# Kernel tuning notes

Hardware: AMD Instinct MI355X
Metric: run time of the kernel (lower is better)

## Reference

```python
import jax, jax.numpy as jnp
import numpy as np

LAM = 5.0
NUM_STEPS = 100
B, N, D = 8, 1024, 256


def setup_inputs() -> dict:
    key = jax.random.key(0)
    k1, k2 = jax.random.split(key)
    fA = jax.random.normal(k1, (B, N, D), dtype=jnp.float32)
    fB = jax.random.normal(k2, (B, N, D), dtype=jnp.float32)
    dustbin = jnp.zeros((1,), dtype=jnp.float32)  # learned dustbin score, init 0.0
    return {"fA": fA, "fB": fB, "dustbin": dustbin}


def _l2_normalize(x, eps=1e-12):
    # matches tf.math.l2_normalize: x / sqrt(max(sum(x^2), eps))
    return x * jax.lax.rsqrt(jnp.maximum(jnp.sum(x * x, axis=-1, keepdims=True), eps))


def _forward(fA, fB, dustbin):
    b, n, _ = fA.shape
    fA = _l2_normalize(fA)
    fB = _l2_normalize(fB)
    Sij = jnp.einsum('bnd,bmd->bnm', fA, fB)  # (B, N, N)
    # augment with dustbin row/col -> (B, N+1, N+1)
    row = dustbin * jnp.ones((b, 1, n), Sij.dtype)
    col = dustbin * jnp.ones((b, n + 1, 1), Sij.dtype)
    S_aug = jnp.concatenate([jnp.concatenate([Sij, row], axis=1), col], axis=2)
    Cij = jnp.clip(-S_aug, -15.0 / LAM, 15.0 / LAM)
    # marginals: [1,...,1, N] for both rows and cols
    ab = jnp.concatenate([jnp.ones((n,), Sij.dtype), jnp.full((1,), float(n), Sij.dtype)])[None, :]  # (1, N+1)
    P = jnp.exp(-LAM * Cij)
    P = P / jnp.sum(P, axis=(1, 2), keepdims=True)

    def step(P, _):
        # NOTE: row_sum/col_sum both computed from the SAME P, as in the TF code
        row_sum = jnp.sum(P, axis=1)  # (B, N+1)
        col_sum = jnp.sum(P, axis=2)  # (B, N+1)
        P = P * (ab / col_sum)[:, :, None]
        P = P * (ab / row_sum)[:, None, :]
        return P, None

    P, _ = jax.lax.scan(jax.checkpoint(step), P, None, length=NUM_STEPS)
    return P


def reference(fA, fB, dustbin):
    return _forward(fA, fB, dustbin)
```

## Files before the change

### kernel.cpp

```cpp
#include <hip/hip_runtime.h>
#include <math.h>
#include <stdint.h>

#define NB 8
#define NN 1024
#define DD 256
#define NP1 1025
#define LDC 1028
#define NSTEPS 100

__global__ __launch_bounds__(256) void norm_kernel(const float* __restrict__ fA,
                                                   const float* __restrict__ fB,
                                                   float* __restrict__ invA,
                                                   float* __restrict__ invB) {
  int gw = (blockIdx.x * 256 + threadIdx.x) >> 6;
  int lane = threadIdx.x & 63;
  const float* src;
  float* dst;
  int row;
  if (gw < NB * NN) { src = fA; dst = invA; row = gw; }
  else              { src = fB; dst = invB; row = gw - NB * NN; }
  float4 v = *(const float4*)(src + (size_t)row * DD + lane * 4);
  double ss = (double)v.x * v.x + (double)v.y * v.y + (double)v.z * v.z + (double)v.w * v.w;
#pragma unroll
  for (int o = 32; o; o >>= 1) ss += __shfl_xor(ss, o, 64);
  if (lane == 0) dst[row] = (float)(1.0 / sqrt(fmax(ss, 1e-12)));
}

__global__ __launch_bounds__(256) void gemm_exp_kernel(const float* __restrict__ fA,
                                                       const float* __restrict__ fB,
                                                       const float* __restrict__ invA,
                                                       const float* __restrict__ invB,
                                                       float* __restrict__ P0,
                                                       double* __restrict__ partZ) {
  const int id = blockIdx.x;
  const int b = id & 7;
  const int tile = id >> 3;
  const int bx = tile & 15, by = tile >> 4;
  const int row0 = by * 64, col0 = bx * 64;
  const int tid = threadIdx.x;
  const int tx = tid & 15, ty = tid >> 4;
  __shared__ __align__(16) float As[16][68];
  __shared__ __align__(16) float Bs[16][68];
  __shared__ double zred[256];
  float acc[4][4] = {{0.f}};
  const int lm = tid >> 2, kq = (tid & 3) << 2;
  const float sa = invA[b * NN + row0 + lm];
  const float sb = invB[b * NN + col0 + lm];
  const float* pA = fA + (size_t)(b * NN + row0 + lm) * DD + kq;
  const float* pB = fB + (size_t)(b * NN + col0 + lm) * DD + kq;
  for (int k0 = 0; k0 < DD; k0 += 16) {
    const float4 a4 = *(const float4*)(pA + k0);
    const float4 b4 = *(const float4*)(pB + k0);
    As[kq + 0][lm] = a4.x * sa; As[kq + 1][lm] = a4.y * sa;
    As[kq + 2][lm] = a4.z * sa; As[kq + 3][lm] = a4.w * sa;
    Bs[kq + 0][lm] = b4.x * sb; Bs[kq + 1][lm] = b4.y * sb;
    Bs[kq + 2][lm] = b4.z * sb; Bs[kq + 3][lm] = b4.w * sb;
    __syncthreads();
#pragma unroll
    for (int kk = 0; kk < 16; ++kk) {
      const float4 av = *(const float4*)&As[kk][ty * 4];
      const float4 bv = *(const float4*)&Bs[kk][tx * 4];
      const float ar[4] = {av.x, av.y, av.z, av.w};
      const float br[4] = {bv.x, bv.y, bv.z, bv.w};
#pragma unroll
      for (int a = 0; a < 4; ++a)
#pragma unroll
        for (int e = 0; e < 4; ++e)
          acc[a][e] = fmaf(ar[a], br[e], acc[a][e]);
    }
    __syncthreads();
  }
  double zs = 0.0;
#pragma unroll
  for (int a = 0; a < 4; ++a)
#pragma unroll
    for (int e = 0; e < 4; ++e) {
      const float S = acc[a][e];
      const float C = fminf(fmaxf(-S, -3.0f), 3.0f);
      const float p = expf(-5.0f * C);
      acc[a][e] = p;
      zs += (double)p;
    }
  {
    float* P0b = P0 + (size_t)b * NN * NN;
#pragma unroll
    for (int a = 0; a < 4; ++a) {
      float4 v;
      v.x = acc[a][0]; v.y = acc[a][1]; v.z = acc[a][2]; v.w = acc[a][3];
      *(float4*)(P0b + (size_t)(row0 + ty * 4 + a) * NN + col0 + tx * 4) = v;
    }
  }
  zred[tid] = zs;
  __syncthreads();
#pragma unroll
  for (int o = 128; o; o >>= 1) {
    if (tid < o) zred[tid] += zred[tid + o];
    __syncthreads();
  }
  if (tid == 0) partZ[(b * 16 + by) * 16 + bx] = zred[0];
}

__global__ __launch_bounds__(256) void init_rc_kernel(const double* __restrict__ partZ,
                                                      float* __restrict__ r0,
                                                      double* __restrict__ Binit,
                                                      double* __restrict__ Bzero) {
  const int b = blockIdx.x, tid = threadIdx.x;
  __shared__ double red[256];
  red[tid] = partZ[b * 256 + tid];
  __syncthreads();
#pragma unroll
  for (int o = 128; o; o >>= 1) {
    if (tid < o) red[tid] += red[tid + o];
    __syncthreads();
  }
  const double Z = red[0];
  const float rv = (float)(1.0 / Z);
  for (int i = tid; i < NP1; i += 256) {
    r0[b * NP1 + i] = rv;
    Binit[b * NP1 + i] = (i == NN) ? (double)NN : 1.0;
    Bzero[b * NP1 + i] = 0.0;
  }
}

__global__ __launch_bounds__(512, 4) void step_kernel(const float* __restrict__ P0,
                                                      const float* __restrict__ dustbin,
                                                      const float* __restrict__ rin,
                                                      float* __restrict__ rout,
                                                      const double* __restrict__ Bprev,
                                                      double* __restrict__ Bacc,
                                                      double* __restrict__ Bzero) {
  const int id = blockIdx.x;
  const int b = id & 7;
  const int s = id >> 3;
  const int tid = threadIdx.x;
  const int lane = tid & 63;
  const int wv = tid >> 6;
  const bool desig = (s == 63);

  __shared__ __align__(16) float c_f[NN];
  __shared__ __align__(16) float part_lds[8][NN];
  __shared__ double wredR[8];
  __shared__ double wredC[8];
  __shared__ double cN_sh;

  const float d = dustbin[0];
  const float dv = expf(-5.0f * fminf(fmaxf(-d, -3.0f), 3.0f));
  const double dv_d = (double)dv;

  const float* P0b = P0 + (size_t)b * NN * NN;
  const float* rv_in = rin + b * NP1;
  const int rowA = s * 16 + wv;
  const int rowB = rowA + 8;
  const float wA = rv_in[rowA];
  const float wB = rv_in[rowB];
  const float4* pA4 = (const float4*)(P0b + (size_t)rowA * NN);
  const float4* pB4 = (const float4*)(P0b + (size_t)rowB * NN);

  float4 a4[4], b4[4];
#pragma unroll
  for (int k = 0; k < 4; ++k) {
    a4[k] = pA4[lane + (k << 6)];
    b4[k] = pB4[lane + (k << 6)];
  }

  if (tid < 17) {
    const int idx = id * 17 + tid;
    if (idx < NB * NP1) Bzero[idx] = 0.0;
  }
  const double* Bp = Bprev + b * NP1;
  for (int j = tid; j < NN; j += 512) c_f[j] = (float)(1.0 / Bp[j]);
  if (tid == 0) cN_sh = (double)NN / Bp[NN];
  __syncthreads();
  const double cN = cN_sh;

  double dotA = 0.0, dotB = 0.0;
  float4 pk[4];
#pragma unroll
  for (int k = 0; k < 4; ++k) {
    const int j4 = lane + (k << 6);
    const float4 cc = ((const float4*)c_f)[j4];
    dotA += (double)a4[k].x * (double)cc.x + (double)a4[k].y * (double)cc.y +
            (double)a4[k].z * (double)cc.z + (double)a4[k].w * (double)cc.w;
    dotB += (double)b4[k].x * (double)cc.x + (double)b4[k].y * (double)cc.y +
            (double)b4[k].z * (double)cc.z + (double)b4[k].w * (double)cc.w;
    pk[k].x = fmaf(wA, a4[k].x, wB * b4[k].x);
    pk[k].y = fmaf(wA, a4[k].y, wB * b4[k].y);
    pk[k].z = fmaf(wA, a4[k].z, wB * b4[k].z);
    pk[k].w = fmaf(wA, a4[k].w, wB * b4[k].w);
  }
#pragma unroll
  for (int o = 32; o; o >>= 1) {
    dotA += __shfl_xor(dotA, o, 64);
    dotB += __shfl_xor(dotB, o, 64);
  }
  dotA += dv_d * cN;
  dotB += dv_d * cN;
  if (lane == 0) {
    float* ro = rout + b * NP1;
    ro[rowA] = (float)(1.0 / dotA);
    ro[rowB] = (float)(1.0 / dotB);
    wredR[wv] = (double)wA + (double)wB;
  }
  {
    float4* pl4 = (float4*)&part_lds[wv][0];
#pragma unroll
    for (int k = 0; k < 4; ++k) pl4[lane + (k << 6)] = pk[k];
  }
  {
    double cs = (double)c_f[tid] + (double)c_f[tid + 512];
#pragma unroll
    for (int o = 32; o; o >>= 1) cs += __shfl_xor(cs, o, 64);
    if (lane == 0) wredC[wv] = cs;
  }
  __syncthreads();

  const float rN = rv_in[NN];
  const float rNdv = rN * dv;
  double* Ba = Bacc + b * NP1;
  for (int j = tid; j < NN; j += 512) {
    float s0 = ((part_lds[0][j] + part_lds[1][j]) + (part_lds[2][j] + part_lds[3][j])) +
               ((part_lds[4][j] + part_lds[5][j]) + (part_lds[6][j] + part_lds[7][j]));
    if (desig) s0 += rNdv;
    atomicAdd(Ba + j, (double)s0);
  }
  if (tid == 0) {
    double rsum = ((wredR[0] + wredR[1]) + (wredR[2] + wredR[3])) +
                  ((wredR[4] + wredR[5]) + (wredR[6] + wredR[7]));
    if (desig) rsum += (double)rN;
    atomicAdd(Ba + NN, dv_d * rsum);
    if (desig) {
      const double sc = ((wredC[0] + wredC[1]) + (wredC[2] + wredC[3])) +
                        ((wredC[4] + wredC[5]) + (wredC[6] + wredC[7])) + cN;
      rout[b * NP1 + NN] = (float)((double)NN / (dv_d * sc));
    }
  }
}

__global__ __launch_bounds__(256) void cfinal_kernel(const double* __restrict__ Bfin,
                                                     float* __restrict__ cfin) {
  const int b = blockIdx.x;
  for (int j = threadIdx.x; j < NP1; j += 256)
    cfin[b * LDC + j] = (float)(((j == NN) ? (double)NN : 1.0) / Bfin[b * NP1 + j]);
}

__global__ __launch_bounds__(256) void finalize_kernel(const float* __restrict__ P0,
                                                       const float* __restrict__ dustbin,
                                                       float* __restrict__ Pout,
                                                       const float* __restrict__ rfin,
                                                       const float* __restrict__ cfin) {
  const int bi = blockIdx.x;
  const int b = bi & 7, i = bi >> 3;
  const int tid = threadIdx.x;
  const float d = dustbin[0];
  const float dv = expf(-5.0f * fminf(fmaxf(-d, -3.0f), 3.0f));
  const float4* cv = (const float4*)(cfin + b * LDC);
  const float cN = cfin[b * LDC + NN];
  float* dst = Pout + (size_t)b * NP1 * NP1 + (size_t)i * NP1;
  const float4 c = cv[tid];
  if (i < NN) {
    const float rv = rfin[b * NP1 + i];
    const float4 p = ((const float4*)(P0 + ((size_t)b * NN + i) * NN))[tid];
    dst[tid * 4 + 0] = rv * p.x * c.x;
    dst[tid * 4 + 1] = rv * p.y * c.y;
    dst[tid * 4 + 2] = rv * p.z * c.z;
    dst[tid * 4 + 3] = rv * p.w * c.w;
    if (tid == 0) dst[NN] = rv * dv * cN;
  } else {
    const float rv = rfin[b * NP1 + NN];
    dst[tid * 4 + 0] = rv * dv * c.x;
    dst[tid * 4 + 1] = rv * dv * c.y;
    dst[tid * 4 + 2] = rv * dv * c.z;
    dst[tid * 4 + 3] = rv * dv * c.w;
    if (tid == 0) dst[NN] = rv * dv * cN;
  }
}

extern "C" void kernel_launch(void* const* d_in, const int* in_sizes, int n_in,
                              void* d_out, int out_size, void* d_ws, size_t ws_size,
                              hipStream_t stream) {
  const float* fA = (const float*)d_in[0];
  const float* fB = (const float*)d_in[1];
  const float* dustbin = (const float*)d_in[2];

  float* Pout = (float*)d_out;

  float* P0 = (float*)d_ws;
  float* rbuf = P0 + (size_t)NB * NN * NN;
  float* cfin = rbuf + 2 * NB * NP1;
  double* Bbuf = (double*)(((uintptr_t)(cfin + NB * LDC) + 15) & ~(uintptr_t)15);
  double* partZ = Bbuf + 3 * NB * NP1;
  float* invA = (float*)(partZ + NB * 256);
  float* invB = invA + NB * NN;

  norm_kernel<<<4096, 256, 0, stream>>>(fA, fB, invA, invB);
  gemm_exp_kernel<<<2048, 256, 0, stream>>>(fA, fB, invA, invB, P0, partZ);
  init_rc_kernel<<<NB, 256, 0, stream>>>(partZ, rbuf, Bbuf + 2 * NB * NP1, Bbuf);

  for (int t = 0; t < NSTEPS; ++t) {
    float* rin = rbuf + (t & 1) * NB * NP1;
    float* rout = rbuf + ((t + 1) & 1) * NB * NP1;
    double* Bprev = Bbuf + ((t + 2) % 3) * NB * NP1;
    double* Bacc = Bbuf + (t % 3) * NB * NP1;
    double* Bzero = Bbuf + ((t + 1) % 3) * NB * NP1;
    step_kernel<<<512, 512, 0, stream>>>(P0, dustbin, rin, rout, Bprev, Bacc, Bzero);
  }

  cfinal_kernel<<<NB, 256, 0, stream>>>(Bbuf, cfin);
  finalize_kernel<<<NB * NP1, 256, 0, stream>>>(P0, dustbin, Pout, rbuf, cfin);
}
```

Before: 994.0 us.

## Retile step kernel so each thread owns a column strip across eight rows

The step kernel changes from a whole-row-per-wave mapping to a column-strip mapping. Each wave covers 256 columns over 8 rows, and each thread keeps four column scales in registers. This drops the per-block LDS column-scale array and the 8x1024 partial-sum buffer, and shrinks the column reduction to one LDS exchange between two halves. In exchange, row dot products now need eight 64-lane double shuffle reductions per wave plus a cross-wave combine, and there are more double atomics per thread. Register pressure goes up under the 512,4 launch bounds.

```diff
diff --git a/kernel.cpp b/kernel.cpp
--- a/kernel.cpp
+++ b/kernel.cpp
@@ -136,12 +136,16 @@
   const int tid = threadIdx.x;
   const int lane = tid & 63;
   const int wv = tid >> 6;
+  const int wq = wv & 3;
+  const int wh = wv >> 2;
   const bool desig = (s == 63);
-
-  __shared__ __align__(16) float c_f[NN];
-  __shared__ __align__(16) float part_lds[8][NN];
-  __shared__ double wredR[8];
-  __shared__ double wredC[8];
+  const int row0 = s * 16;
+  const int col0 = wq * 256 + lane * 4;
+
+  __shared__ __align__(16) float qlds[1024];
+  __shared__ double dred[16][4];
+  __shared__ double csum_lds[4];
+  __shared__ double rs_lds[2];
   __shared__ double cN_sh;
 
   const float d = dustbin[0];
@@ -150,90 +154,91 @@
 
   const float* P0b = P0 + (size_t)b * NN * NN;
   const float* rv_in = rin + b * NP1;
-  const int rowA = s * 16 + wv;
-  const int rowB = rowA + 8;
-  const float wA = rv_in[rowA];
-  const float wB = rv_in[rowB];
-  const float4* pA4 = (const float4*)(P0b + (size_t)rowA * NN);
-  const float4* pB4 = (const float4*)(P0b + (size_t)rowB * NN);
-
-  float4 a4[4], b4[4];
-#pragma unroll
-  for (int k = 0; k < 4; ++k) {
-    a4[k] = pA4[lane + (k << 6)];
-    b4[k] = pB4[lane + (k << 6)];
-  }
+  const double* Bp = Bprev + b * NP1;
+
+  float4 p[8];
+#pragma unroll
+  for (int q = 0; q < 8; ++q)
+    p[q] = *(const float4*)(P0b + (size_t)(row0 + wh * 8 + q) * NN + col0);
+  const double bd0 = Bp[col0 + 0], bd1 = Bp[col0 + 1];
+  const double bd2 = Bp[col0 + 2], bd3 = Bp[col0 + 3];
+  float rw[8];
+#pragma unroll
+  for (int q = 0; q < 8; ++q) rw[q] = rv_in[row0 + wh * 8 + q];
 
   if (tid < 17) {
     const int idx = id * 17 + tid;
     if (idx < NB * NP1) Bzero[idx] = 0.0;
   }
-  const double* Bp = Bprev + b * NP1;
-  for (int j = tid; j < NN; j += 512) c_f[j] = (float)(1.0 / Bp[j]);
   if (tid == 0) cN_sh = (double)NN / Bp[NN];
+
+  const float cf0 = (float)(1.0 / bd0), cf1 = (float)(1.0 / bd1);
+  const float cf2 = (float)(1.0 / bd2), cf3 = (float)(1.0 / bd3);
+  const double c0 = (double)cf0, c1 = (double)cf1;
+  const double c2 = (double)cf2, c3 = (double)cf3;
+
+  double dq[8];
+  float4 qacc = {0.f, 0.f, 0.f, 0.f};
+#pragma unroll
+  for (int q = 0; q < 8; ++q) {
+    dq[q] = (double)p[q].x * c0 + (double)p[q].y * c1 +
+            (double)p[q].z * c2 + (double)p[q].w * c3;
+    qacc.x = fmaf(rw[q], p[q].x, qacc.x);
+    qacc.y = fmaf(rw[q], p[q].y, qacc.y);
+    qacc.z = fmaf(rw[q], p[q].z, qacc.z);
+    qacc.w = fmaf(rw[q], p[q].w, qacc.w);
+  }
+#pragma unroll
+  for (int o = 32; o; o >>= 1) {
+#pragma unroll
+    for (int q = 0; q < 8; ++q) dq[q] += __shfl_xor(dq[q], o, 64);
+  }
+  if (lane == 0) {
+#pragma unroll
+    for (int q = 0; q < 8; ++q) dred[wh * 8 + q][wq] = dq[q];
+  }
+  if (wh == 0) {
+    double cs = (c0 + c1) + (c2 + c3);
+#pragma unroll
+    for (int o = 32; o; o >>= 1) cs += __shfl_xor(cs, o, 64);
+    if (lane == 0) csum_lds[wq] = cs;
+    *(float4*)&qlds[col0] = qacc;
+  }
+  if ((wv == 0 || wv == 4) && lane == 0) {
+    double rs = 0.0;
+#pragma unroll
+    for (int q = 0; q < 8; ++q) rs += (double)rw[q];
+    rs_lds[wh] = rs;
+  }
   __syncthreads();
+
   const double cN = cN_sh;
-
-  double dotA = 0.0, dotB = 0.0;
-  float4 pk[4];
-#pragma unroll
-  for (int k = 0; k < 4; ++k) {
-    const int j4 = lane + (k << 6);
-    const float4 cc = ((const float4*)c_f)[j4];
-    dotA += (double)a4[k].x * (double)cc.x + (double)a4[k].y * (double)cc.y +
-            (double)a4[k].z * (double)cc.z + (double)a4[k].w * (double)cc.w;
-    dotB += (double)b4[k].x * (double)cc.x + (double)b4[k].y * (double)cc.y +
-            (double)b4[k].z * (double)cc.z + (double)b4[k].w * (double)cc.w;
-    pk[k].x = fmaf(wA, a4[k].x, wB * b4[k].x);
-    pk[k].y = fmaf(wA, a4[k].y, wB * b4[k].y);
-    pk[k].z = fmaf(wA, a4[k].z, wB * b4[k].z);
-    pk[k].w = fmaf(wA, a4[k].w, wB * b4[k].w);
-  }
-#pragma unroll
-  for (int o = 32; o; o >>= 1) {
-    dotA += __shfl_xor(dotA, o, 64);
-    dotB += __shfl_xor(dotB, o, 64);
-  }
-  dotA += dv_d * cN;
-  dotB += dv_d * cN;
-  if (lane == 0) {
-    float* ro = rout + b * NP1;
-    ro[rowA] = (float)(1.0 / dotA);
-    ro[rowB] = (float)(1.0 / dotB);
-    wredR[wv] = (double)wA + (double)wB;
-  }
-  {
-    float4* pl4 = (float4*)&part_lds[wv][0];
-#pragma unroll
-    for (int k = 0; k < 4; ++k) pl4[lane + (k << 6)] = pk[k];
-  }
-  {
-    double cs = (double)c_f[tid] + (double)c_f[tid + 512];
-#pragma unroll
-    for (int o = 32; o; o >>= 1) cs += __shfl_xor(cs, o, 64);
-    if (lane == 0) wredC[wv] = cs;
-  }
-  __syncthreads();
-
-  const float rN = rv_in[NN];
-  const float rNdv = rN * dv;
+  float* ro = rout + b * NP1;
   double* Ba = Bacc + b * NP1;
-  for (int j = tid; j < NN; j += 512) {
-    float s0 = ((part_lds[0][j] + part_lds[1][j]) + (part_lds[2][j] + part_lds[3][j])) +
-               ((part_lds[4][j] + part_lds[5][j]) + (part_lds[6][j] + part_lds[7][j]));
-    if (desig) s0 += rNdv;
-    atomicAdd(Ba + j, (double)s0);
-  }
-  if (tid == 0) {
-    double rsum = ((wredR[0] + wredR[1]) + (wredR[2] + wredR[3])) +
-                  ((wredR[4] + wredR[5]) + (wredR[6] + wredR[7]));
-    if (desig) rsum += (double)rN;
+  if (tid < 16) {
+    const double dot = ((dred[tid][0] + dred[tid][1]) +
+                        (dred[tid][2] + dred[tid][3])) + dv_d * cN;
+    ro[row0 + tid] = (float)(1.0 / dot);
+  } else if (tid == 16) {
+    double rsum = rs_lds[0] + rs_lds[1];
+    if (desig) rsum += (double)rv_in[NN];
     atomicAdd(Ba + NN, dv_d * rsum);
+  } else if (tid == 17 && desig) {
+    const double sc = ((csum_lds[0] + csum_lds[1]) +
+                       (csum_lds[2] + csum_lds[3])) + cN;
+    ro[NN] = (float)((double)NN / (dv_d * sc));
+  }
+  if (wh == 1) {
+    float4 qo = *(const float4*)&qlds[col0];
+    qo.x += qacc.x; qo.y += qacc.y; qo.z += qacc.z; qo.w += qacc.w;
     if (desig) {
-      const double sc = ((wredC[0] + wredC[1]) + (wredC[2] + wredC[3])) +
-                        ((wredC[4] + wredC[5]) + (wredC[6] + wredC[7])) + cN;
-      rout[b * NP1 + NN] = (float)((double)NN / (dv_d * sc));
+      const float rNdv = rv_in[NN] * dv;
+      qo.x += rNdv; qo.y += rNdv; qo.z += rNdv; qo.w += rNdv;
     }
+    atomicAdd(Ba + col0 + 0, (double)qo.x);
+    atomicAdd(Ba + col0 + 1, (double)qo.y);
+    atomicAdd(Ba + col0 + 2, (double)qo.z);
+    atomicAdd(Ba + col0 + 3, (double)qo.w);
   }
 }
 
```

New measurement: 2.376 ms. 139% more time.
